# Kernel optimization log

Measured on AMD Instinct MI355X. Metric: run time of the kernel, lower is better.

## Reference

```python
import jax, jax.numpy as jnp
import numpy as np

# dims
B, L, DM, DS, K, E, DFF, R = 16, 1024, 512, 16, 4, 2, 2048, 32
DI = DM  # expand = 1 -> d_inner == d_model

PARAM_NAMES = ['m_in_w','m_conv_w','m_conv_b','m_xproj_w','m_dt_w','m_dt_b','m_A_log','m_D','m_out_w']


def setup_inputs() -> dict:
    key = jax.random.key(0)
    ks = iter(jax.random.split(key, 32))
    def rn(shape, scale=0.02):
        return jax.random.normal(next(ks), shape, dtype=jnp.float32) * scale
    inp = {
        'x': jax.random.normal(next(ks), (B, L, DM), dtype=jnp.float32),
        # per layer (E) and per direction (2: forward mamba, reversed mamba)
        'm_in_w':   rn((E, 2, 2 * DI, DM)),
        'm_conv_w': rn((E, 2, DI, K), 0.1),
        'm_conv_b': jnp.zeros((E, 2, DI), jnp.float32),
        'm_xproj_w': rn((E, 2, R + 2 * DS, DI)),
        'm_dt_w':   rn((E, 2, DI, R), 0.1),
        'm_dt_b':   jnp.full((E, 2, DI), -4.0, jnp.float32) + rn((E, 2, DI), 0.1),
        'm_A_log':  jnp.log(jnp.broadcast_to(jnp.arange(1, DS + 1, dtype=jnp.float32), (E, 2, DI, DS))),
        'm_D':      jnp.ones((E, 2, DI), jnp.float32),
        'm_out_w':  rn((E, 2, DM, DI)),
        # FFN (1x1 convs == linears) and norms per layer
        'ff_w1': rn((E, DFF, DM)), 'ff_b1': jnp.zeros((E, DFF), jnp.float32),
        'ff_w2': rn((E, DM, DFF)), 'ff_b2': jnp.zeros((E, DM), jnp.float32),
        'ln1_g': jnp.ones((E, DM), jnp.float32), 'ln1_b': jnp.zeros((E, DM), jnp.float32),
        'ln2_g': jnp.ones((E, DM), jnp.float32), 'ln2_b': jnp.zeros((E, DM), jnp.float32),
        'lnf_g': jnp.ones((DM,), jnp.float32),   'lnf_b': jnp.zeros((DM,), jnp.float32),
    }
    return inp


def layer_norm(x, g, b, eps=1e-5):
    mu = x.mean(-1, keepdims=True)
    var = ((x - mu) ** 2).mean(-1, keepdims=True)
    return (x - mu) * jax.lax.rsqrt(var + eps) * g + b


def mamba(x, in_w, conv_w, conv_b, xproj_w, dt_w, dt_b, A_log, Dp, out_w):
    # x: (B, L, DM)
    Bsz, Lseq, _ = x.shape
    xz = x @ in_w.T                       # (B, L, 2*DI)
    xc, z = jnp.split(xz, 2, axis=-1)
    # depthwise causal conv1d (kernel K, left pad K-1, truncate to L)
    xp = jnp.pad(xc, ((0, 0), (K - 1, 0), (0, 0)))
    xc = sum(conv_w[:, k] * xp[:, k:k + Lseq, :] for k in range(K)) + conv_b
    xc = jax.nn.silu(xc)
    dbl = xc @ xproj_w.T                  # (B, L, R + 2*DS)
    dt, Bm, Cm = dbl[..., :R], dbl[..., R:R + DS], dbl[..., R + DS:]
    dt = jax.nn.softplus(dt @ dt_w.T + dt_b)  # (B, L, DI)
    A = -jnp.exp(A_log)                   # (DI, DS)

    def step(h, inputs):
        dt_t, B_t, C_t, x_t = inputs      # (B,DI) (B,DS) (B,DS) (B,DI)
        dA = jnp.exp(dt_t[..., None] * A)             # (B, DI, DS)
        h = dA * h + (dt_t * x_t)[..., None] * B_t[:, None, :]
        y = jnp.einsum('bds,bs->bd', h, C_t)
        return h, y

    xs = (dt.transpose(1, 0, 2), Bm.transpose(1, 0, 2), Cm.transpose(1, 0, 2), xc.transpose(1, 0, 2))
    h0 = jnp.zeros((Bsz, DI, DS), dtype=x.dtype)
    _, ys = jax.lax.scan(step, h0, xs)    # ys: (L, B, DI)
    y = ys.transpose(1, 0, 2) + xc * Dp
    y = y * jax.nn.silu(z)
    return y @ out_w.T                    # (B, L, DM)


def _forward(x, m_in_w, m_conv_w, m_conv_b, m_xproj_w, m_dt_w, m_dt_b, m_A_log, m_D, m_out_w,
             ff_w1, ff_b1, ff_w2, ff_b2, ln1_g, ln1_b, ln2_g, ln2_b, lnf_g, lnf_b):
    packs = (m_in_w, m_conv_w, m_conv_b, m_xproj_w, m_dt_w, m_dt_b, m_A_log, m_D, m_out_w)
    for e in range(E):
        p_fwd = tuple(a[e, 0] for a in packs)
        p_rev = tuple(a[e, 1] for a in packs)
        # bidirectional mamba mixing (second block sees the time-flipped sequence)
        new_x = mamba(x, *p_fwd) + mamba(x[:, ::-1], *p_rev)[:, ::-1]
        x = x + new_x
        xn = layer_norm(x, ln1_g[e], ln1_b[e])
        y = jax.nn.gelu(xn @ ff_w1[e].T + ff_b1[e], approximate=False)
        y = y @ ff_w2[e].T + ff_b2[e]
        x = layer_norm(xn + y, ln2_g[e], ln2_b[e])
    return layer_norm(x, lnf_g, lnf_b)


def reference(x, m_in_w, m_conv_w, m_conv_b, m_xproj_w, m_dt_w, m_dt_b, m_A_log, m_D, m_out_w,
              ff_w1, ff_b1, ff_w2, ff_b2, ln1_g, ln1_b, ln2_g, ln2_b, lnf_g, lnf_b):
    return _forward(x, m_in_w, m_conv_w, m_conv_b, m_xproj_w, m_dt_w, m_dt_b, m_A_log, m_D, m_out_w,
                    ff_w1, ff_b1, ff_w2, ff_b2, ln1_g, ln1_b, ln2_g, ln2_b, lnf_g, lnf_b)
```

## Files before the change

### kernel.cpp

```cpp
#include <hip/hip_runtime.h>
#include <hip/hip_bf16.h>
#include <math.h>

#define DEVI __device__ __forceinline__

namespace {
constexpr int kL   = 1024;
constexpr int kDM  = 512;
constexpr int kDS  = 16;
constexpr int kDFF = 2048;
constexpr int kR   = 32;
constexpr int kDI  = 512;
constexpr int kB   = 16;
constexpr int kM   = kB * kL;
constexpr int kNC  = 32;
constexpr int kCH  = kL / kNC;
}

typedef __attribute__((ext_vector_type(8))) short short8;
typedef __attribute__((ext_vector_type(4))) float f32x4;

DEVI float silu_f(float x)     { return x / (1.f + __expf(-x)); }
DEVI float softplus_f(float x) { return fmaxf(x, 0.f) + log1pf(__expf(-fabsf(x))); }
DEVI float gelu_f(float x)     { return 0.5f * x * (1.f + erff(x * 0.70710678118654752f)); }

DEVI unsigned short f2bf(float f) {
    unsigned int u = __float_as_uint(f);
    return (unsigned short)((u + 0x7fffu + ((u >> 16) & 1u)) >> 16);
}
DEVI float bf2f(unsigned short u) {
    return __uint_as_float(((unsigned int)u) << 16);
}
DEVI uint2 pack4(float4 v) {
    uint2 p;
    p.x = (unsigned int)f2bf(v.x) | ((unsigned int)f2bf(v.y) << 16);
    p.y = (unsigned int)f2bf(v.z) | ((unsigned int)f2bf(v.w) << 16);
    return p;
}

typedef const __attribute__((address_space(1))) unsigned int* gas1;
typedef __attribute__((address_space(3))) unsigned int* las3;
DEVI void gload16(const unsigned short* g, unsigned short* l) {
    __builtin_amdgcn_global_load_lds((gas1)g, (las3)l, 16, 0, 0);
}

struct WCvtArgs { const float* src[6]; unsigned int end[6]; };

__global__ __launch_bounds__(256) void cvt_weights_k(
    WCvtArgs a, unsigned short* __restrict__ dst)
{
    unsigned int i = (blockIdx.x * 256 + threadIdx.x) * 4;
    if (i >= a.end[5]) return;
    int j = 0;
    while (i >= a.end[j]) ++j;
    unsigned int base = j ? a.end[j - 1] : 0;
    float4 v = *(const float4*)&a.src[j][i - base];
    *(uint2*)&dst[i] = pack4(v);
}

__global__ __launch_bounds__(256) void init_x_k(
    const float* __restrict__ x, float* __restrict__ xo,
    unsigned short* __restrict__ xb)
{
    size_t i = (size_t)(blockIdx.x * 256 + threadIdx.x) * 4;
    float4 v = *(const float4*)&x[i];
    *(float4*)&xo[i] = v;
    *(uint2*)&xb[i] = pack4(v);
}

template <int BM, int EPI, typename CT>
__global__ __launch_bounds__(512, 2) void gemm8(
    const unsigned short* __restrict__ A, int lda, size_t zA,
    const unsigned short* __restrict__ W, size_t zW,
    CT* __restrict__ C, int ldc, size_t zC,
    const float* __restrict__ biasb, int zBias,
    const float* __restrict__ add, int Kd)
{
    static_assert(BM == 128 || BM == 256, "");
    constexpr int MF = BM / 32;
    constexpr int AL = BM / 64;
    __shared__ alignas(16) unsigned short As[2][BM * 64];
    __shared__ alignas(16) unsigned short Ws[2][256 * 64];

    const int z = blockIdx.z;
    A += (size_t)z * zA; W += (size_t)z * zW; C += (size_t)z * zC;
    const float* bias = biasb ? biasb + (size_t)z * zBias : nullptr;

    const int gx = gridDim.x;
    int flat = blockIdx.y * gx + blockIdx.x;
    const int total = gx * gridDim.y;
    if ((total & 7) == 0) { int q = total >> 3; flat = (flat & 7) * q + (flat >> 3); }
    const int bx = flat % gx;
    const int by = flat / gx;
    const int row0 = by * BM, col0 = bx * 256;

    const int tid = threadIdx.x, lane = tid & 63, wv = tid >> 6;
    const int wm = wv >> 2, wn = wv & 3;

    f32x4 acc[MF][4];
#pragma unroll
    for (int m = 0; m < MF; ++m)
#pragma unroll
        for (int n = 0; n < 4; ++n) acc[m][n] = (f32x4){0.f, 0.f, 0.f, 0.f};

    const int srow = tid >> 3;
    const int sk   = (((tid & 7) ^ (srow & 7)) * 8);
    const unsigned short* Ag = A + (size_t)(row0 + srow) * lda + sk;
    const unsigned short* Wg = W + (size_t)(col0 + srow) * Kd + sk;
    const int ldso = srow * 64 + (tid & 7) * 8;

    auto stage = [&](int buf, int k0) {
#pragma unroll
        for (int i = 0; i < AL; ++i)
            gload16(Ag + (size_t)(64 * i) * lda + k0, &As[buf][ldso + i * 4096]);
#pragma unroll
        for (int i = 0; i < 4; ++i)
            gload16(Wg + (size_t)(64 * i) * Kd + k0, &Ws[buf][ldso + i * 4096]);
    };

    const int nt = Kd / 64;
    stage(0, 0);
    if (nt > 1) stage(1, 64);

    const int fr = lane & 15;
    const int cb = lane >> 4;

    for (int t = 0; t < nt; ++t) {
        if (t + 1 < nt) {
            if constexpr (BM == 256) asm volatile("s_waitcnt vmcnt(8)" ::: "memory");
            else                     asm volatile("s_waitcnt vmcnt(6)" ::: "memory");
        } else {
            asm volatile("s_waitcnt vmcnt(0)" ::: "memory");
        }
        __builtin_amdgcn_s_barrier();
        __builtin_amdgcn_sched_barrier(0);

        const int cur = t & 1;
        __builtin_amdgcn_s_setprio(1);
#pragma unroll
        for (int kh = 0; kh < 2; ++kh) {
            short8 af[MF], bf[4];
#pragma unroll
            for (int m = 0; m < MF; ++m) {
                int r = wm * (BM / 2) + m * 16 + fr;
                af[m] = *(const short8*)
                    &As[cur][r * 64 + ((((kh << 2) | cb) ^ (r & 7)) << 3)];
            }
#pragma unroll
            for (int n = 0; n < 4; ++n) {
                int r = wn * 64 + n * 16 + fr;
                bf[n] = *(const short8*)
                    &Ws[cur][r * 64 + ((((kh << 2) | cb) ^ (r & 7)) << 3)];
            }
#pragma unroll
            for (int m = 0; m < MF; ++m)
#pragma unroll
                for (int n = 0; n < 4; ++n)
                    acc[m][n] = __builtin_amdgcn_mfma_f32_16x16x32_bf16(
                        af[m], bf[n], acc[m][n], 0, 0, 0);
        }
        __builtin_amdgcn_s_setprio(0);

        __builtin_amdgcn_sched_barrier(0);
        __builtin_amdgcn_s_barrier();
        __builtin_amdgcn_sched_barrier(0);
        if (t + 2 < nt) stage(cur, (t + 2) * 64);
    }

    const int cr = (lane >> 4) * 4;
#pragma unroll
    for (int m = 0; m < MF; ++m) {
#pragma unroll
        for (int n = 0; n < 4; ++n) {
            int cn = col0 + wn * 64 + n * 16 + fr;
#pragma unroll
            for (int r = 0; r < 4; ++r) {
                int rr = row0 + wm * (BM / 2) + m * 16 + cr + r;
                size_t idx = (size_t)rr * ldc + cn;
                float v = acc[m][n][r];
                if constexpr (EPI == 0) {
                    if constexpr (__is_same(CT, unsigned short)) C[idx] = f2bf(v);
                    else C[idx] = v;
                } else if constexpr (EPI == 3) {
                    C[idx] = f2bf(gelu_f(v + bias[cn]));
                } else {
                    C[idx] = v + bias[cn] + add[idx];
                }
            }
        }
    }
}

template <int EPI, int BN, typename CT>
__global__ __launch_bounds__(256) void gemm_bf16(
    const unsigned short* __restrict__ A, int lda, size_t zA,
    const unsigned short* __restrict__ W, size_t zW,
    CT* __restrict__ C, int ldc, size_t zC,
    const float* __restrict__ biasb, int zBias,
    unsigned short* __restrict__ auxb, size_t zAux, int Kd)
{
    static_assert(BN == 64 || BN == 128, "");
    constexpr int NF = BN / 32;
    __shared__ alignas(16) unsigned short As[2][128 * 32];
    __shared__ alignas(16) unsigned short Ws[2][BN * 32];

    const int z = blockIdx.z;
    A += (size_t)z * zA; W += (size_t)z * zW; C += (size_t)z * zC;
    const float* bias = biasb ? biasb + (size_t)z * zBias : nullptr;
    unsigned short* aux = auxb ? auxb + (size_t)z * zAux : nullptr;

    const int gx = gridDim.x;
    int flat = blockIdx.y * gx + blockIdx.x;
    const int total = gx * gridDim.y;
    if ((total & 7) == 0) {
        int q = total >> 3;
        flat = (flat & 7) * q + (flat >> 3);
    }
    const int bx = flat % gx;
    const int by = flat / gx;

    const int tid  = threadIdx.x;
    const int lane = tid & 63;
    const int wv   = tid >> 6;
    const int wm   = wv >> 1;
    const int wn   = wv & 1;
    const int row0 = by * 128;
    const int col0 = bx * BN;

    f32x4 acc[4][NF];
#pragma unroll
    for (int m = 0; m < 4; ++m)
#pragma unroll
        for (int n = 0; n < NF; ++n) acc[m][n] = (f32x4){0.f, 0.f, 0.f, 0.f};

    const int sr  = tid >> 2;
    const int scw = (((tid & 3) ^ ((tid >> 3) & 3)) * 8);
    const unsigned short* Ag = A + (size_t)(row0 + sr) * lda + scw;
    const unsigned short* Wg = W + (size_t)(col0 + sr) * Kd + scw;

    auto stage = [&](int buf, int k0) {
        gload16(Ag + k0, &As[buf][tid * 8]);
        gload16(Ag + (size_t)64 * lda + k0, &As[buf][2048 + tid * 8]);
        gload16(Wg + k0, &Ws[buf][tid * 8]);
        if (BN == 128)
            gload16(Wg + (size_t)64 * Kd + k0, &Ws[buf][2048 + tid * 8]);
    };

    const int nt = Kd / 32;
    stage(0, 0);
    __syncthreads();

    const int fr  = lane & 15;
    const int sw8 = (((lane >> 4) ^ ((fr >> 1) & 3)) * 8);

    int cur = 0;
    for (int t = 0; t < nt; ++t) {
        if (t + 1 < nt) stage(cur ^ 1, (t + 1) * 32);
        short8 af[4], bf[NF];
#pragma unroll
        for (int m = 0; m < 4; ++m)
            af[m] = *(const short8*)&As[cur][(wm * 64 + m * 16 + fr) * 32 + sw8];
#pragma unroll
        for (int n = 0; n < NF; ++n)
            bf[n] = *(const short8*)&Ws[cur][(wn * (BN / 2) + n * 16 + fr) * 32 + sw8];
        __builtin_amdgcn_s_setprio(1);
#pragma unroll
        for (int m = 0; m < 4; ++m)
#pragma unroll
            for (int n = 0; n < NF; ++n)
                acc[m][n] = __builtin_amdgcn_mfma_f32_16x16x32_bf16(
                    af[m], bf[n], acc[m][n], 0, 0, 0);
        __builtin_amdgcn_s_setprio(0);
        __syncthreads();
        cur ^= 1;
    }

    const int cr = (lane >> 4) * 4;
#pragma unroll
    for (int m = 0; m < 4; ++m) {
#pragma unroll
        for (int n = 0; n < NF; ++n) {
            int cn = col0 + wn * (BN / 2) + n * 16 + fr;
#pragma unroll
            for (int r = 0; r < 4; ++r) {
                int rr = row0 + wm * 64 + m * 16 + cr + r;
                size_t idx = (size_t)rr * ldc + cn;
                float v = acc[m][n][r];
                if constexpr (EPI == 1) {
                    float sp = softplus_f(v + bias[cn]);
                    if constexpr (__is_same(CT, unsigned short)) C[idx] = f2bf(sp);
                    else C[idx] = sp;
                } else {
                    C[idx] = v;
                    if (cn < 32) aux[(size_t)rr * 32 + cn] = f2bf(v);
                }
            }
        }
    }
}

__global__ __launch_bounds__(128) void conv_silu_k(
    const unsigned short* __restrict__ xz2, unsigned short* __restrict__ xcb,
    const float* __restrict__ wb, const float* __restrict__ biasb)
{
    const int task = blockIdx.x * 128 + threadIdx.x;
    const int g   = task & 63;
    const int c   = (task >> 6) & 31;
    const int b   = (task >> 11) & 15;
    const int dir = (task >> 15) & 1;
    const int d0  = g * 8;

    const unsigned short* xzd = xz2 + (size_t)dir * 1024 + (size_t)b * kL * 2048 + d0;
    unsigned short* xc = xcb + (size_t)dir * kM * kDI + (size_t)b * kL * kDI + d0;
    const float* w    = wb + (size_t)dir * 2048;
    const float* bias = biasb + (size_t)dir * 512;

    float wk[4][8];
#pragma unroll
    for (int k = 0; k < 4; ++k)
#pragma unroll
        for (int j = 0; j < 8; ++j)
            wk[k][j] = w[(d0 + j) * 4 + (dir ? 3 - k : k)];
    float bs[8];
#pragma unroll
    for (int j = 0; j < 8; ++j) bs[j] = bias[d0 + j];

    const int t0 = c * 32;
    const int rbase = dir ? t0 : t0 - 3;

    auto loadrow = [&](int t, float* o) {
        if (t < 0 || t >= kL) {
#pragma unroll
            for (int j = 0; j < 8; ++j) o[j] = 0.f;
            return;
        }
        uint4 p = *(const uint4*)&xzd[(size_t)t * 2048];
        o[0] = bf2f((unsigned short)(p.x & 0xffff));
        o[1] = bf2f((unsigned short)(p.x >> 16));
        o[2] = bf2f((unsigned short)(p.y & 0xffff));
        o[3] = bf2f((unsigned short)(p.y >> 16));
        o[4] = bf2f((unsigned short)(p.z & 0xffff));
        o[5] = bf2f((unsigned short)(p.z >> 16));
        o[6] = bf2f((unsigned short)(p.w & 0xffff));
        o[7] = bf2f((unsigned short)(p.w >> 16));
    };

    float x0[8], x1[8], x2[8];
    loadrow(rbase + 0, x0);
    loadrow(rbase + 1, x1);
    loadrow(rbase + 2, x2);

#pragma unroll 4
    for (int i = 0; i < 32; ++i) {
        float x3[8];
        loadrow(rbase + 3 + i, x3);
        unsigned short o[8];
#pragma unroll
        for (int j = 0; j < 8; ++j) {
            float v = bs[j];
            v = fmaf(wk[0][j], x0[j], v);
            v = fmaf(wk[1][j], x1[j], v);
            v = fmaf(wk[2][j], x2[j], v);
            v = fmaf(wk[3][j], x3[j], v);
            o[j] = f2bf(silu_f(v));
        }
        *(uint4*)&xc[(size_t)(t0 + i) * kDI] = *(uint4*)o;
#pragma unroll
        for (int j = 0; j < 8; ++j) { x0[j] = x1[j]; x1[j] = x2[j]; x2[j] = x3[j]; }
    }
}

__global__ __launch_bounds__(256) void scan_chunk(
    const unsigned short* __restrict__ dtb2, const unsigned short* __restrict__ xcb2,
    const float* __restrict__ dbl2, const float* __restrict__ A_logb,
    float* __restrict__ S2, float* __restrict__ sdt2)
{
    int dir = blockIdx.y;
    const unsigned short* dtb = dtb2 + (size_t)dir * kM * kDI;
    const unsigned short* xcb = xcb2 + (size_t)dir * kM * kDI;
    const float* dbl = dbl2 + (size_t)dir * kM * 64;
    const float* A_log = A_logb + (size_t)dir * 8192;
    float* S   = S2 + (size_t)dir * (kB * kNC * kDS * kDI);
    float* sdt = sdt2 + (size_t)dir * (kB * kNC * kDI);

    int blk  = blockIdx.x;
    int dblk = blk & 1;
    int c    = (blk >> 1) & (kNC - 1);
    int b    = blk >> 6;
    int d    = dblk * 256 + threadIdx.x;

    const float* al = A_log + d * kDS;
    float A[16];
#pragma unroll
    for (int s = 0; s < 16; ++s) A[s] = -__expf(al[s]);

    float h[16];
#pragma unroll
    for (int s = 0; s < 16; ++s) h[s] = 0.f;
    float sum = 0.f;

#pragma unroll 2
    for (int i = 0; i < kCH; ++i) {
        int p   = c * kCH + i;
        int t   = dir ? (kL - 1 - p) : p;
        int row = b * kL + t;
        float dt = bf2f(dtb[(size_t)row * kDI + d]);
        float xv = bf2f(xcb[(size_t)row * kDI + d]);
        sum += dt;
        float dx = dt * xv;
        const float4* bp = (const float4*)(dbl + (size_t)row * 64 + kR);
        float4 b0 = bp[0], b1 = bp[1], b2 = bp[2], b3 = bp[3];
        float Bv[16] = {b0.x, b0.y, b0.z, b0.w, b1.x, b1.y, b1.z, b1.w,
                        b2.x, b2.y, b2.z, b2.w, b3.x, b3.y, b3.z, b3.w};
#pragma unroll
        for (int s = 0; s < 16; ++s) {
            float q = __expf(dt * A[s]);
            h[s] = fmaf(q, h[s], dx * Bv[s]);
        }
    }
    size_t base = (size_t)(b * kNC + c) * kDS * kDI + d;
#pragma unroll
    for (int s = 0; s < 16; ++s) S[base + s * kDI] = h[s];
    sdt[(size_t)(b * kNC + c) * kDI + d] = sum;
}

__global__ __launch_bounds__(256) void scan_carry(
    float* __restrict__ S2, const float* __restrict__ sdt2,
    const float* __restrict__ A_logb)
{
    int dir = blockIdx.y;
    float* S = S2 + (size_t)dir * (kB * kNC * kDS * kDI);
    const float* sdt = sdt2 + (size_t)dir * (kB * kNC * kDI);
    const float* A_log = A_logb + (size_t)dir * 8192;

    int g = blockIdx.x * 256 + threadIdx.x;
    int d = g & (kDI - 1);
    int s = (g >> 9) & 15;
    int b = g >> 13;

    float A = -__expf(A_log[d * kDS + s]);
    float h = 0.f;
#pragma unroll
    for (int c = 0; c < kNC; ++c) {
        size_t base = ((size_t)(b * kNC + c) * kDS + s) * kDI + d;
        float sv = S[base];
        float sd = sdt[(size_t)(b * kNC + c) * kDI + d];
        S[base] = h;
        h = fmaf(__expf(sd * A), h, sv);
    }
}

__global__ __launch_bounds__(256) void scan_emit(
    const unsigned short* __restrict__ dtb2, const unsigned short* __restrict__ xcb2,
    const float* __restrict__ dbl2, const float* __restrict__ A_logb,
    const float* __restrict__ h0v2, const float* __restrict__ Dpb,
    const unsigned short* __restrict__ xz2, unsigned short* __restrict__ yb2)
{
    int dir = blockIdx.y;
    const unsigned short* dtb = dtb2 + (size_t)dir * kM * kDI;
    const unsigned short* xcb = xcb2 + (size_t)dir * kM * kDI;
    const float* dbl = dbl2 + (size_t)dir * kM * 64;
    const float* A_log = A_logb + (size_t)dir * 8192;
    const float* h0v = h0v2 + (size_t)dir * (kB * kNC * kDS * kDI);
    const float* Dp = Dpb + (size_t)dir * 512;
    const unsigned short* zg = xz2 + (size_t)dir * 1024 + 512;
    unsigned short* yb = yb2 + (size_t)dir * kM * kDI;

    int blk  = blockIdx.x;
    int dblk = blk & 1;
    int c    = (blk >> 1) & (kNC - 1);
    int b    = blk >> 6;
    int d    = dblk * 256 + threadIdx.x;

    const float* al = A_log + d * kDS;
    float A[16];
#pragma unroll
    for (int s = 0; s < 16; ++s) A[s] = -__expf(al[s]);
    float Dd = Dp[d];

    size_t hbase = (size_t)(b * kNC + c) * kDS * kDI + d;
    float h[16];
#pragma unroll
    for (int s = 0; s < 16; ++s) h[s] = h0v[hbase + s * kDI];

#pragma unroll 2
    for (int i = 0; i < kCH; ++i) {
        int p   = c * kCH + i;
        int t   = dir ? (kL - 1 - p) : p;
        int row = b * kL + t;
        float dt = bf2f(dtb[(size_t)row * kDI + d]);
        float xv = bf2f(xcb[(size_t)row * kDI + d]);
        float dx = dt * xv;
        const float4* bp = (const float4*)(dbl + (size_t)row * 64 + kR);
        float4 b0 = bp[0], b1 = bp[1], b2 = bp[2], b3 = bp[3];
        const float4* cp = (const float4*)(dbl + (size_t)row * 64 + kR + kDS);
        float4 c0 = cp[0], c1 = cp[1], c2 = cp[2], c3 = cp[3];
        float Bv[16] = {b0.x, b0.y, b0.z, b0.w, b1.x, b1.y, b1.z, b1.w,
                        b2.x, b2.y, b2.z, b2.w, b3.x, b3.y, b3.z, b3.w};
        float Cv[16] = {c0.x, c0.y, c0.z, c0.w, c1.x, c1.y, c1.z, c1.w,
                        c2.x, c2.y, c2.z, c2.w, c3.x, c3.y, c3.z, c3.w};
        float y = 0.f;
#pragma unroll
        for (int s = 0; s < 16; ++s) {
            float q = __expf(dt * A[s]);
            h[s] = fmaf(q, h[s], dx * Bv[s]);
            y = fmaf(h[s], Cv[s], y);
        }
        y += xv * Dd;
        float z = bf2f(zg[(size_t)row * 2048 + d]);
        yb[(size_t)row * kDI + d] = f2bf(y * silu_f(z));
    }
}

__global__ __launch_bounds__(128) void ln_k(
    const float* __restrict__ in, const float* __restrict__ a0,
    const float* __restrict__ a1,
    const float* __restrict__ g, const float* __restrict__ bb,
    float* __restrict__ out, unsigned short* __restrict__ outbf)
{
    int row = blockIdx.x;
    int tid = threadIdx.x;
    size_t off = (size_t)row * kDM + tid * 4;
    float4 v = *(const float4*)&in[off];
    if (a0) {
        float4 u = *(const float4*)&a0[off];
        float4 w = *(const float4*)&a1[off];
        v.x += u.x + w.x; v.y += u.y + w.y; v.z += u.z + w.z; v.w += u.w + w.w;
    }
    float s1 = v.x + v.y + v.z + v.w;
    float s2 = v.x * v.x + v.y * v.y + v.z * v.z + v.w * v.w;
#pragma unroll
    for (int o = 32; o >= 1; o >>= 1) {
        s1 += __shfl_xor(s1, o);
        s2 += __shfl_xor(s2, o);
    }
    __shared__ float red[4];
    if ((tid & 63) == 0) { red[(tid >> 6) * 2] = s1; red[(tid >> 6) * 2 + 1] = s2; }
    __syncthreads();
    s1 = red[0] + red[2];
    s2 = red[1] + red[3];
    float mu  = s1 * (1.f / kDM);
    float var = s2 * (1.f / kDM) - mu * mu;
    float rs  = rsqrtf(var + 1e-5f);
    int cn = tid * 4;
    float4 gv = *(const float4*)&g[cn];
    float4 bv = *(const float4*)&bb[cn];
    float4 o;
    o.x = (v.x - mu) * rs * gv.x + bv.x;
    o.y = (v.y - mu) * rs * gv.y + bv.y;
    o.z = (v.z - mu) * rs * gv.z + bv.z;
    o.w = (v.w - mu) * rs * gv.w + bv.w;
    *(float4*)&out[off] = o;
    if (outbf)
        *(uint2*)&outbf[off] = pack4(o);
}

extern "C" void kernel_launch(void* const* d_in, const int* in_sizes, int n_in,
                              void* d_out, int out_size, void* d_ws, size_t ws_size,
                              hipStream_t stream)
{
    const float* x_in    = (const float*)d_in[0];
    const float* in_w    = (const float*)d_in[1];
    const float* conv_w  = (const float*)d_in[2];
    const float* conv_b  = (const float*)d_in[3];
    const float* xproj_w = (const float*)d_in[4];
    const float* dt_w    = (const float*)d_in[5];
    const float* dt_b    = (const float*)d_in[6];
    const float* A_log   = (const float*)d_in[7];
    const float* Dp      = (const float*)d_in[8];
    const float* out_w   = (const float*)d_in[9];
    const float* ff_w1   = (const float*)d_in[10];
    const float* ff_b1   = (const float*)d_in[11];
    const float* ff_w2   = (const float*)d_in[12];
    const float* ff_b2   = (const float*)d_in[13];
    const float* ln1_g   = (const float*)d_in[14];
    const float* ln1_b   = (const float*)d_in[15];
    const float* ln2_g   = (const float*)d_in[16];
    const float* ln2_b   = (const float*)d_in[17];
    const float* lnf_g   = (const float*)d_in[18];
    const float* lnf_b   = (const float*)d_in[19];

    float* ws = (float*)d_ws;
    unsigned short* wsb = (unsigned short*)d_ws;

    unsigned short* wb_in  = wsb;
    unsigned short* wb_xp  = wsb + 2097152;
    unsigned short* wb_out = wsb + 2228224;
    unsigned short* wb_f1  = wsb + 3276800;
    unsigned short* wb_f2  = wsb + 5373952;
    unsigned short* wb_dt  = wsb + 7471104;

    constexpr size_t A0 = 3768320;
    unsigned short* xbf  = (unsigned short*)(ws + A0);
    unsigned short* xz2  = (unsigned short*)(ws + A0 + 4194304);
    unsigned short* xcb2 = (unsigned short*)(ws + A0 + 20971520);
    unsigned short* yb2  = (unsigned short*)(ws + A0 + 29360128);
    float*          Sb2  = ws + A0 + 37748736;
    unsigned short* dtb2 = (unsigned short*)(ws + A0 + 46137344);
    float*          dbl2 = ws + A0 + 54525952;
    unsigned short* dtin2= (unsigned short*)(ws + A0 + 56623104);
    float*          sdt2 = ws + A0 + 57147392;
    float*          o2   = ws + A0 + 37748736;
    float*          xn   = ws + A0;
    unsigned short* xnbf = (unsigned short*)(ws + A0 + 8388608);
    unsigned short* Hb   = (unsigned short*)(ws + A0 + 12582912);
    float*          t2   = ws + A0 + 29360128;

    float* xcur = (float*)d_out;
    dim3 thr(256);

    WCvtArgs wa;
    wa.src[0] = in_w;    wa.end[0] = 2097152;
    wa.src[1] = xproj_w; wa.end[1] = 2228224;
    wa.src[2] = out_w;   wa.end[2] = 3276800;
    wa.src[3] = ff_w1;   wa.end[3] = 5373952;
    wa.src[4] = ff_w2;   wa.end[4] = 7471104;
    wa.src[5] = dt_w;    wa.end[5] = 7536640;
    cvt_weights_k<<<dim3(7536640 / 1024), thr, 0, stream>>>(wa, wsb);
    init_x_k<<<dim3(8192), thr, 0, stream>>>(x_in, xcur, xbf);

    for (int e = 0; e < 2; ++e) {
        gemm8<256, 0, unsigned short><<<dim3(8, 64, 1), dim3(512), 0, stream>>>(
            xbf, 512, 0, wb_in + (size_t)e * 1048576, 0, xz2, 2048, 0,
            nullptr, 0, nullptr, 512);
        conv_silu_k<<<dim3(512), dim3(128), 0, stream>>>(
            xz2, xcb2, conv_w + (size_t)e * 4096, conv_b + (size_t)e * 1024);
        gemm_bf16<5, 64, float><<<dim3(1, 128, 2), thr, 0, stream>>>(
            xcb2, 512, (size_t)kM * 512, wb_xp + (size_t)e * 65536, 32768,
            dbl2, 64, (size_t)kM * 64, nullptr, 0, dtin2, (size_t)kM * 32, 512);
        gemm_bf16<1, 128, unsigned short><<<dim3(4, 128, 2), thr, 0, stream>>>(
            dtin2, 32, (size_t)kM * 32, wb_dt + (size_t)e * 32768, 16384,
            dtb2, 512, (size_t)kM * 512, dt_b + (size_t)e * 1024, 512,
            nullptr, 0, 32);
        scan_chunk<<<dim3(kB * kNC * 2, 2), thr, 0, stream>>>(
            dtb2, xcb2, dbl2, A_log + (size_t)e * 16384, Sb2, sdt2);
        scan_carry<<<dim3(512, 2), thr, 0, stream>>>(
            Sb2, sdt2, A_log + (size_t)e * 16384);
        scan_emit<<<dim3(kB * kNC * 2, 2), thr, 0, stream>>>(
            dtb2, xcb2, dbl2, A_log + (size_t)e * 16384, Sb2,
            Dp + (size_t)e * 1024, xz2, yb2);
        gemm8<128, 0, float><<<dim3(2, 128, 2), dim3(512), 0, stream>>>(
            yb2, 512, (size_t)kM * 512, wb_out + (size_t)e * 524288, 262144,
            o2, 512, (size_t)kM * 512, nullptr, 0, nullptr, 512);
        ln_k<<<dim3(kM), dim3(128), 0, stream>>>(
            xcur, o2, o2 + (size_t)kM * 512,
            ln1_g + e * kDM, ln1_b + e * kDM, xn, xnbf);
        gemm8<256, 3, unsigned short><<<dim3(8, 64, 1), dim3(512), 0, stream>>>(
            xnbf, 512, 0, wb_f1 + (size_t)e * 1048576, 0, Hb, 2048, 0,
            ff_b1 + (size_t)e * kDFF, 0, nullptr, 512);
        gemm8<128, 4, float><<<dim3(2, 128, 1), dim3(512), 0, stream>>>(
            Hb, 2048, 0, wb_f2 + (size_t)e * 1048576, 0, t2, 512, 0,
            ff_b2 + (size_t)e * kDM, 0, xn, 2048);
        ln_k<<<dim3(kM), dim3(128), 0, stream>>>(
            t2, nullptr, nullptr, ln2_g + e * kDM, ln2_b + e * kDM, xcur,
            e == 0 ? xbf : nullptr);
    }
    ln_k<<<dim3(kM), dim3(128), 0, stream>>>(
        xcur, nullptr, nullptr, lnf_g, lnf_b, xcur, nullptr);
}
```

Measured before the change: 971.5 us.

## Fuse dt projection into scan kernels and replace big-tile GEMM with smaller tiles

The dt low-rank projection plus softplus is now computed inside scan_chunk and scan_emit from the 32-wide dt input and dt weights. This removes the separate dt GEMM and the full-width dt buffer's write and two reads. At the same time the large 512-thread, 256x256-tile gemm8 kernel is deleted and every big GEMM now uses the smaller 128x128, 256-thread gemm_bf16 kernel, which has simpler double buffering. The cost is that dt is computed twice (once per scan pass), and the large GEMMs may lose data reuse and pipelining depth.

New measurement: 1.095 ms. 12.8% more time.

```diff
diff --git a/kernel.cpp b/kernel.cpp
--- a/kernel.cpp
+++ b/kernel.cpp
@@ -68,114 +68,100 @@
     *(uint2*)&xb[i] = pack4(v);
 }
 
-template <int BM, int EPI, typename CT>
-__global__ __launch_bounds__(512, 2) void gemm8(
+template <int EPI, int BN, typename CT>
+__global__ __launch_bounds__(256) void gemm_bf16(
     const unsigned short* __restrict__ A, int lda, size_t zA,
     const unsigned short* __restrict__ W, size_t zW,
     CT* __restrict__ C, int ldc, size_t zC,
     const float* __restrict__ biasb, int zBias,
-    const float* __restrict__ add, int Kd)
-{
-    static_assert(BM == 128 || BM == 256, "");
-    constexpr int MF = BM / 32;
-    constexpr int AL = BM / 64;
-    __shared__ alignas(16) unsigned short As[2][BM * 64];
-    __shared__ alignas(16) unsigned short Ws[2][256 * 64];
+    const float* __restrict__ add,
+    unsigned short* __restrict__ auxb, size_t zAux, int Kd)
+{
+    static_assert(BN == 64 || BN == 128, "");
+    constexpr int NF = BN / 32;
+    __shared__ alignas(16) unsigned short As[2][128 * 32];
+    __shared__ alignas(16) unsigned short Ws[2][BN * 32];
 
     const int z = blockIdx.z;
     A += (size_t)z * zA; W += (size_t)z * zW; C += (size_t)z * zC;
     const float* bias = biasb ? biasb + (size_t)z * zBias : nullptr;
+    unsigned short* aux = auxb ? auxb + (size_t)z * zAux : nullptr;
 
     const int gx = gridDim.x;
     int flat = blockIdx.y * gx + blockIdx.x;
     const int total = gx * gridDim.y;
-    if ((total & 7) == 0) { int q = total >> 3; flat = (flat & 7) * q + (flat >> 3); }
+    if ((total & 7) == 0) {
+        int q = total >> 3;
+        flat = (flat & 7) * q + (flat >> 3);
+    }
     const int bx = flat % gx;
     const int by = flat / gx;
-    const int row0 = by * BM, col0 = bx * 256;
-
-    const int tid = threadIdx.x, lane = tid & 63, wv = tid >> 6;
-    const int wm = wv >> 2, wn = wv & 3;
-
-    f32x4 acc[MF][4];
-#pragma unroll
-    for (int m = 0; m < MF; ++m)
-#pragma unroll
-        for (int n = 0; n < 4; ++n) acc[m][n] = (f32x4){0.f, 0.f, 0.f, 0.f};
-
-    const int srow = tid >> 3;
-    const int sk   = (((tid & 7) ^ (srow & 7)) * 8);
-    const unsigned short* Ag = A + (size_t)(row0 + srow) * lda + sk;
-    const unsigned short* Wg = W + (size_t)(col0 + srow) * Kd + sk;
-    const int ldso = srow * 64 + (tid & 7) * 8;
+
+    const int tid  = threadIdx.x;
+    const int lane = tid & 63;
+    const int wv   = tid >> 6;
+    const int wm   = wv >> 1;
+    const int wn   = wv & 1;
+    const int row0 = by * 128;
+    const int col0 = bx * BN;
+
+    f32x4 acc[4][NF];
+#pragma unroll
+    for (int m = 0; m < 4; ++m)
+#pragma unroll
+        for (int n = 0; n < NF; ++n) acc[m][n] = (f32x4){0.f, 0.f, 0.f, 0.f};
+
+    const int sr  = tid >> 2;
+    const int scw = (((tid & 3) ^ ((tid >> 3) & 3)) * 8);
+    const unsigned short* Ag = A + (size_t)(row0 + sr) * lda + scw;
+    const unsigned short* Wg = W + (size_t)(col0 + sr) * Kd + scw;
 
     auto stage = [&](int buf, int k0) {
-#pragma unroll
-        for (int i = 0; i < AL; ++i)
-            gload16(Ag + (size_t)(64 * i) * lda + k0, &As[buf][ldso + i * 4096]);
-#pragma unroll
-        for (int i = 0; i < 4; ++i)
-            gload16(Wg + (size_t)(64 * i) * Kd + k0, &Ws[buf][ldso + i * 4096]);
+        gload16(Ag + k0, &As[buf][tid * 8]);
+        gload16(Ag + (size_t)64 * lda + k0, &As[buf][2048 + tid * 8]);
+        gload16(Wg + k0, &Ws[buf][tid * 8]);
+        if (BN == 128)
+            gload16(Wg + (size_t)64 * Kd + k0, &Ws[buf][2048 + tid * 8]);
     };
 
-    const int nt = Kd / 64;
+    const int nt = Kd / 32;
     stage(0, 0);
-    if (nt > 1) stage(1, 64);
-
-    const int fr = lane & 15;
-    const int cb = lane >> 4;
-
+    __syncthreads();
+
+    const int fr  = lane & 15;
+    const int sw8 = (((lane >> 4) ^ ((fr >> 1) & 3)) * 8);
+
+    int cur = 0;
     for (int t = 0; t < nt; ++t) {
-        if (t + 1 < nt) {
-            if constexpr (BM == 256) asm volatile("s_waitcnt vmcnt(8)" ::: "memory");
-            else                     asm volatile("s_waitcnt vmcnt(6)" ::: "memory");
-        } else {
-            asm volatile("s_waitcnt vmcnt(0)" ::: "memory");
-        }
-        __builtin_amdgcn_s_barrier();
-        __builtin_amdgcn_sched_barrier(0);
-
-        const int cur = t & 1;
+        if (t + 1 < nt) stage(cur ^ 1, (t + 1) * 32);
+        short8 af[4], bf[NF];
+#pragma unroll
+        for (int m = 0; m < 4; ++m)
+            af[m] = *(const short8*)&As[cur][(wm * 64 + m * 16 + fr) * 32 + sw8];
+#pragma unroll
+        for (int n = 0; n < NF; ++n)
+            bf[n] = *(const short8*)&Ws[cur][(wn * (BN / 2) + n * 16 + fr) * 32 + sw8];
         __builtin_amdgcn_s_setprio(1);
 #pragma unroll
-        for (int kh = 0; kh < 2; ++kh) {
-            short8 af[MF], bf[4];
-#pragma unroll
-            for (int m = 0; m < MF; ++m) {
-                int r = wm * (BM / 2) + m * 16 + fr;
-                af[m] = *(const short8*)
-                    &As[cur][r * 64 + ((((kh << 2) | cb) ^ (r & 7)) << 3)];
-            }
-#pragma unroll
-            for (int n = 0; n < 4; ++n) {
-                int r = wn * 64 + n * 16 + fr;
-                bf[n] = *(const short8*)
-                    &Ws[cur][r * 64 + ((((kh << 2) | cb) ^ (r & 7)) << 3)];
-            }
-#pragma unroll
-            for (int m = 0; m < MF; ++m)
-#pragma unroll
-                for (int n = 0; n < 4; ++n)
-                    acc[m][n] = __builtin_amdgcn_mfma_f32_16x16x32_bf16(
-                        af[m], bf[n], acc[m][n], 0, 0, 0);
-        }
+        for (int m = 0; m < 4; ++m)
+#pragma unroll
+            for (int n = 0; n < NF; ++n)
+                acc[m][n] = __builtin_amdgcn_mfma_f32_16x16x32_bf16(
+                    af[m], bf[n], acc[m][n], 0, 0, 0);
         __builtin_amdgcn_s_setprio(0);
-
-        __builtin_amdgcn_sched_barrier(0);
-        __builtin_amdgcn_s_barrier();
-        __builtin_amdgcn_sched_barrier(0);
-        if (t + 2 < nt) stage(cur, (t + 2) * 64);
+        __syncthreads();
+        cur ^= 1;
     }
 
     const int cr = (lane >> 4) * 4;
 #pragma unroll
-    for (int m = 0; m < MF; ++m) {
-#pragma unroll
-        for (int n = 0; n < 4; ++n) {
-            int cn = col0 + wn * 64 + n * 16 + fr;
+    for (int m = 0; m < 4; ++m) {
+#pragma unroll
+        for (int n = 0; n < NF; ++n) {
+            int cn = col0 + wn * (BN / 2) + n * 16 + fr;
 #pragma unroll
             for (int r = 0; r < 4; ++r) {
-                int rr = row0 + wm * (BM / 2) + m * 16 + cr + r;
+                int rr = row0 + wm * 64 + m * 16 + cr + r;
                 size_t idx = (size_t)rr * ldc + cn;
                 float v = acc[m][n][r];
                 if constexpr (EPI == 0) {
@@ -183,113 +169,8 @@
                     else C[idx] = v;
                 } else if constexpr (EPI == 3) {
                     C[idx] = f2bf(gelu_f(v + bias[cn]));
-                } else {
+                } else if constexpr (EPI == 4) {
                     C[idx] = v + bias[cn] + add[idx];
-                }
-            }
-        }
-    }
-}
-
-template <int EPI, int BN, typename CT>
-__global__ __launch_bounds__(256) void gemm_bf16(
-    const unsigned short* __restrict__ A, int lda, size_t zA,
-    const unsigned short* __restrict__ W, size_t zW,
-    CT* __restrict__ C, int ldc, size_t zC,
-    const float* __restrict__ biasb, int zBias,
-    unsigned short* __restrict__ auxb, size_t zAux, int Kd)
-{
-    static_assert(BN == 64 || BN == 128, "");
-    constexpr int NF = BN / 32;
-    __shared__ alignas(16) unsigned short As[2][128 * 32];
-    __shared__ alignas(16) unsigned short Ws[2][BN * 32];
-
-    const int z = blockIdx.z;
-    A += (size_t)z * zA; W += (size_t)z * zW; C += (size_t)z * zC;
-    const float* bias = biasb ? biasb + (size_t)z * zBias : nullptr;
-    unsigned short* aux = auxb ? auxb + (size_t)z * zAux : nullptr;
-
-    const int gx = gridDim.x;
-    int flat = blockIdx.y * gx + blockIdx.x;
-    const int total = gx * gridDim.y;
-    if ((total & 7) == 0) {
-        int q = total >> 3;
-        flat = (flat & 7) * q + (flat >> 3);
-    }
-    const int bx = flat % gx;
-    const int by = flat / gx;
-
-    const int tid  = threadIdx.x;
-    const int lane = tid & 63;
-    const int wv   = tid >> 6;
-    const int wm   = wv >> 1;
-    const int wn   = wv & 1;
-    const int row0 = by * 128;
-    const int col0 = bx * BN;
-
-    f32x4 acc[4][NF];
-#pragma unroll
-    for (int m = 0; m < 4; ++m)
-#pragma unroll
-        for (int n = 0; n < NF; ++n) acc[m][n] = (f32x4){0.f, 0.f, 0.f, 0.f};
-
-    const int sr  = tid >> 2;
-    const int scw = (((tid & 3) ^ ((tid >> 3) & 3)) * 8);
-    const unsigned short* Ag = A + (size_t)(row0 + sr) * lda + scw;
-    const unsigned short* Wg = W + (size_t)(col0 + sr) * Kd + scw;
-
-    auto stage = [&](int buf, int k0) {
-        gload16(Ag + k0, &As[buf][tid * 8]);
-        gload16(Ag + (size_t)64 * lda + k0, &As[buf][2048 + tid * 8]);
-        gload16(Wg + k0, &Ws[buf][tid * 8]);
-        if (BN == 128)
-            gload16(Wg + (size_t)64 * Kd + k0, &Ws[buf][2048 + tid * 8]);
-    };
-
-    const int nt = Kd / 32;
-    stage(0, 0);
-    __syncthreads();
-
-    const int fr  = lane & 15;
-    const int sw8 = (((lane >> 4) ^ ((fr >> 1) & 3)) * 8);
-
-    int cur = 0;
-    for (int t = 0; t < nt; ++t) {
-        if (t + 1 < nt) stage(cur ^ 1, (t + 1) * 32);
-        short8 af[4], bf[NF];
-#pragma unroll
-        for (int m = 0; m < 4; ++m)
-            af[m] = *(const short8*)&As[cur][(wm * 64 + m * 16 + fr) * 32 + sw8];
-#pragma unroll
-        for (int n = 0; n < NF; ++n)
-            bf[n] = *(const short8*)&Ws[cur][(wn * (BN / 2) + n * 16 + fr) * 32 + sw8];
-        __builtin_amdgcn_s_setprio(1);
-#pragma unroll
-        for (int m = 0; m < 4; ++m)
-#pragma unroll
-            for (int n = 0; n < NF; ++n)
-                acc[m][n] = __builtin_amdgcn_mfma_f32_16x16x32_bf16(
-                    af[m], bf[n], acc[m][n], 0, 0, 0);
-        __builtin_amdgcn_s_setprio(0);
-        __syncthreads();
-        cur ^= 1;
-    }
-
-    const int cr = (lane >> 4) * 4;
-#pragma unroll
-    for (int m = 0; m < 4; ++m) {
-#pragma unroll
-        for (int n = 0; n < NF; ++n) {
-            int cn = col0 + wn * (BN / 2) + n * 16 + fr;
-#pragma unroll
-            for (int r = 0; r < 4; ++r) {
-                int rr = row0 + wm * 64 + m * 16 + cr + r;
-                size_t idx = (size_t)rr * ldc + cn;
-                float v = acc[m][n][r];
-                if constexpr (EPI == 1) {
-                    float sp = softplus_f(v + bias[cn]);
-                    if constexpr (__is_same(CT, unsigned short)) C[idx] = f2bf(sp);
-                    else C[idx] = sp;
                 } else {
                     C[idx] = v;
                     if (cn < 32) aux[(size_t)rr * 32 + cn] = f2bf(v);
@@ -370,13 +251,63 @@
     }
 }
 
+DEVI void dt_prologue(
+    const unsigned short* __restrict__ dtin,
+    const unsigned short* __restrict__ dtw,
+    float dtbias, int rbase, int dir, int tid,
+    unsigned short* dlds, float* dtv)
+{
+    {
+        int rr = tid >> 3, cc = (tid & 7) * 4;
+        *(uint2*)&dlds[rr * 32 + cc] =
+            *(const uint2*)&dtin[(size_t)(rbase + rr) * 32 + cc];
+    }
+    float wreg[32];
+    {
+        const uint4* wr = (const uint4*)dtw;
+#pragma unroll
+        for (int q = 0; q < 4; ++q) {
+            uint4 p = wr[q];
+            wreg[q * 8 + 0] = bf2f((unsigned short)(p.x & 0xffff));
+            wreg[q * 8 + 1] = bf2f((unsigned short)(p.x >> 16));
+            wreg[q * 8 + 2] = bf2f((unsigned short)(p.y & 0xffff));
+            wreg[q * 8 + 3] = bf2f((unsigned short)(p.y >> 16));
+            wreg[q * 8 + 4] = bf2f((unsigned short)(p.z & 0xffff));
+            wreg[q * 8 + 5] = bf2f((unsigned short)(p.z >> 16));
+            wreg[q * 8 + 6] = bf2f((unsigned short)(p.w & 0xffff));
+            wreg[q * 8 + 7] = bf2f((unsigned short)(p.w >> 16));
+        }
+    }
+    __syncthreads();
+#pragma unroll
+    for (int i = 0; i < 32; ++i) {
+        int li = dir ? (31 - i) : i;
+        const uint4* dr = (const uint4*)&dlds[li * 32];
+        float acc = dtbias;
+#pragma unroll
+        for (int q = 0; q < 4; ++q) {
+            uint4 p = dr[q];
+            acc = fmaf(bf2f((unsigned short)(p.x & 0xffff)), wreg[q * 8 + 0], acc);
+            acc = fmaf(bf2f((unsigned short)(p.x >> 16)),    wreg[q * 8 + 1], acc);
+            acc = fmaf(bf2f((unsigned short)(p.y & 0xffff)), wreg[q * 8 + 2], acc);
+            acc = fmaf(bf2f((unsigned short)(p.y >> 16)),    wreg[q * 8 + 3], acc);
+            acc = fmaf(bf2f((unsigned short)(p.z & 0xffff)), wreg[q * 8 + 4], acc);
+            acc = fmaf(bf2f((unsigned short)(p.z >> 16)),    wreg[q * 8 + 5], acc);
+            acc = fmaf(bf2f((unsigned short)(p.w & 0xffff)), wreg[q * 8 + 6], acc);
+            acc = fmaf(bf2f((unsigned short)(p.w >> 16)),    wreg[q * 8 + 7], acc);
+        }
+        dtv[i] = softplus_f(acc);
+    }
+}
+
 __global__ __launch_bounds__(256) void scan_chunk(
-    const unsigned short* __restrict__ dtb2, const unsigned short* __restrict__ xcb2,
+    const unsigned short* __restrict__ dtin2, const unsigned short* __restrict__ xcb2,
     const float* __restrict__ dbl2, const float* __restrict__ A_logb,
+    const unsigned short* __restrict__ dtwb, const float* __restrict__ dtbb,
     float* __restrict__ S2, float* __restrict__ sdt2)
 {
     int dir = blockIdx.y;
-    const unsigned short* dtb = dtb2 + (size_t)dir * kM * kDI;
+    const unsigned short* dtin = dtin2 + (size_t)dir * kM * 32;
     const unsigned short* xcb = xcb2 + (size_t)dir * kM * kDI;
     const float* dbl = dbl2 + (size_t)dir * kM * 64;
     const float* A_log = A_logb + (size_t)dir * 8192;
@@ -389,6 +320,12 @@
     int b    = blk >> 6;
     int d    = dblk * 256 + threadIdx.x;
 
+    __shared__ unsigned short dlds[32 * 32];
+    int rbase = b * kL + (dir ? (kL - 32 * (c + 1)) : c * 32);
+    float dtv[32];
+    dt_prologue(dtin, dtwb + (size_t)dir * 16384 + d * 32,
+                dtbb[dir * 512 + d], rbase, dir, threadIdx.x, dlds, dtv);
+
     const float* al = A_log + d * kDS;
     float A[16];
 #pragma unroll
@@ -404,7 +341,7 @@
         int p   = c * kCH + i;
         int t   = dir ? (kL - 1 - p) : p;
         int row = b * kL + t;
-        float dt = bf2f(dtb[(size_t)row * kDI + d]);
+        float dt = dtv[i];
         float xv = bf2f(xcb[(size_t)row * kDI + d]);
         sum += dt;
         float dx = dt * xv;
@@ -451,13 +388,14 @@
 }
 
 __global__ __launch_bounds__(256) void scan_emit(
-    const unsigned short* __restrict__ dtb2, const unsigned short* __restrict__ xcb2,
+    const unsigned short* __restrict__ dtin2, const unsigned short* __restrict__ xcb2,
     const float* __restrict__ dbl2, const float* __restrict__ A_logb,
+    const unsigned short* __restrict__ dtwb, const float* __restrict__ dtbb,
     const float* __restrict__ h0v2, const float* __restrict__ Dpb,
     const unsigned short* __restrict__ xz2, unsigned short* __restrict__ yb2)
 {
     int dir = blockIdx.y;
-    const unsigned short* dtb = dtb2 + (size_t)dir * kM * kDI;
+    const unsigned short* dtin = dtin2 + (size_t)dir * kM * 32;
     const unsigned short* xcb = xcb2 + (size_t)dir * kM * kDI;
     const float* dbl = dbl2 + (size_t)dir * kM * 64;
     const float* A_log = A_logb + (size_t)dir * 8192;
@@ -472,6 +410,12 @@
     int b    = blk >> 6;
     int d    = dblk * 256 + threadIdx.x;
 
+    __shared__ unsigned short dlds[32 * 32];
+    int rbase = b * kL + (dir ? (kL - 32 * (c + 1)) : c * 32);
+    float dtv[32];
+    dt_prologue(dtin, dtwb + (size_t)dir * 16384 + d * 32,
+                dtbb[dir * 512 + d], rbase, dir, threadIdx.x, dlds, dtv);
+
     const float* al = A_log + d * kDS;
     float A[16];
 #pragma unroll
@@ -488,7 +432,7 @@
         int p   = c * kCH + i;
         int t   = dir ? (kL - 1 - p) : p;
         int row = b * kL + t;
-        float dt = bf2f(dtb[(size_t)row * kDI + d]);
+        float dt = dtv[i];
         float xv = bf2f(xcb[(size_t)row * kDI + d]);
         float dx = dt * xv;
         const float4* bp = (const float4*)(dbl + (size_t)row * 64 + kR);
@@ -596,7 +540,6 @@
     unsigned short* xcb2 = (unsigned short*)(ws + A0 + 20971520);
     unsigned short* yb2  = (unsigned short*)(ws + A0 + 29360128);
     float*          Sb2  = ws + A0 + 37748736;
-    unsigned short* dtb2 = (unsigned short*)(ws + A0 + 46137344);
     float*          dbl2 = ws + A0 + 54525952;
     unsigned short* dtin2= (unsigned short*)(ws + A0 + 56623104);
     float*          sdt2 = ws + A0 + 57147392;
@@ -620,37 +563,36 @@
     init_x_k<<<dim3(8192), thr, 0, stream>>>(x_in, xcur, xbf);
 
     for (int e = 0; e < 2; ++e) {
-        gemm8<256, 0, unsigned short><<<dim3(8, 64, 1), dim3(512), 0, stream>>>(
+        gemm_bf16<0, 128, unsigned short><<<dim3(16, 128), thr, 0, stream>>>(
             xbf, 512, 0, wb_in + (size_t)e * 1048576, 0, xz2, 2048, 0,
-            nullptr, 0, nullptr, 512);
+            nullptr, 0, nullptr, nullptr, 0, 512);
         conv_silu_k<<<dim3(512), dim3(128), 0, stream>>>(
             xz2, xcb2, conv_w + (size_t)e * 4096, conv_b + (size_t)e * 1024);
         gemm_bf16<5, 64, float><<<dim3(1, 128, 2), thr, 0, stream>>>(
             xcb2, 512, (size_t)kM * 512, wb_xp + (size_t)e * 65536, 32768,
-            dbl2, 64, (size_t)kM * 64, nullptr, 0, dtin2, (size_t)kM * 32, 512);
-        gemm_bf16<1, 128, unsigned short><<<dim3(4, 128, 2), thr, 0, stream>>>(
-            dtin2, 32, (size_t)kM * 32, wb_dt + (size_t)e * 32768, 16384,
-            dtb2, 512, (size_t)kM * 512, dt_b + (size_t)e * 1024, 512,
-            nullptr, 0, 32);
+            dbl2, 64, (size_t)kM * 64, nullptr, 0, nullptr,
+            dtin2, (size_t)kM * 32, 512);
         scan_chunk<<<dim3(kB * kNC * 2, 2), thr, 0, stream>>>(
-            dtb2, xcb2, dbl2, A_log + (size_t)e * 16384, Sb2, sdt2);
+            dtin2, xcb2, dbl2, A_log + (size_t)e * 16384,
+            wb_dt + (size_t)e * 32768, dt_b + (size_t)e * 1024, Sb2, sdt2);
         scan_carry<<<dim3(512, 2), thr, 0, stream>>>(
             Sb2, sdt2, A_log + (size_t)e * 16384);
         scan_emit<<<dim3(kB * kNC * 2, 2), thr, 0, stream>>>(
-            dtb2, xcb2, dbl2, A_log + (size_t)e * 16384, Sb2,
+            dtin2, xcb2, dbl2, A_log + (size_t)e * 16384,
+            wb_dt + (size_t)e * 32768, dt_b + (size_t)e * 1024, Sb2,
             Dp + (size_t)e * 1024, xz2, yb2);
-        gemm8<128, 0, float><<<dim3(2, 128, 2), dim3(512), 0, stream>>>(
+        gemm_bf16<0, 128, float><<<dim3(4, 128, 2), thr, 0, stream>>>(
             yb2, 512, (size_t)kM * 512, wb_out + (size_t)e * 524288, 262144,
-            o2, 512, (size_t)kM * 512, nullptr, 0, nullptr, 512);
+            o2, 512, (size_t)kM * 512, nullptr, 0, nullptr, nullptr, 0, 512);
         ln_k<<<dim3(kM), dim3(128), 0, stream>>>(
             xcur, o2, o2 + (size_t)kM * 512,
             ln1_g + e * kDM, ln1_b + e * kDM, xn, xnbf);
-        gemm8<256, 3, unsigned short><<<dim3(8, 64, 1), dim3(512), 0, stream>>>(
+        gemm_bf16<3, 128, unsigned short><<<dim3(16, 128), thr, 0, stream>>>(
             xnbf, 512, 0, wb_f1 + (size_t)e * 1048576, 0, Hb, 2048, 0,
-            ff_b1 + (size_t)e * kDFF, 0, nullptr, 512);
-        gemm8<128, 4, float><<<dim3(2, 128, 1), dim3(512), 0, stream>>>(
+            ff_b1 + (size_t)e * kDFF, 0, nullptr, nullptr, 0, 512);
+        gemm_bf16<4, 128, float><<<dim3(4, 128), thr, 0, stream>>>(
             Hb, 2048, 0, wb_f2 + (size_t)e * 1048576, 0, t2, 512, 0,
-            ff_b2 + (size_t)e * kDM, 0, xn, 2048);
+            ff_b2 + (size_t)e * kDM, 0, xn, nullptr, 0, 2048);
         ln_k<<<dim3(kM), dim3(128), 0, stream>>>(
             t2, nullptr, nullptr, ln2_g + e * kDM, ln2_b + e * kDM, xcur,
             e == 0 ? xbf : nullptr);
```
